# Optimization experiments

Measured on AMD Instinct MI355X. Metric: run time of the kernel, lower is better.

Reference implementation:

```python
import jax, jax.numpy as jnp
import numpy as np

N = 100000
E = 3200000
D_IN = 128
H = 32   # 2 * out_channels
OUT = 16 # out_channels


def _glorot(key, shape):
    lim = np.sqrt(6.0 / (shape[0] + shape[1]))
    return jax.random.uniform(key, shape, jnp.float32, -lim, lim)


def setup_inputs() -> dict:
    key = jax.random.key(0)
    ks = jax.random.split(key, 8)
    x = jax.random.normal(ks[0], (N, D_IN), jnp.float32)
    edge_index = jax.random.randint(ks[1], (2, E), 0, N, jnp.int64)
    W1 = _glorot(ks[2], (D_IN, H));  b1 = jnp.zeros((H,), jnp.float32)
    Wm = _glorot(ks[3], (H, OUT));   bm = jnp.zeros((OUT,), jnp.float32)
    Wv = _glorot(ks[4], (H, 1));     bv = jnp.zeros((1,), jnp.float32)
    return {"x": x, "edge_index": edge_index,
            "W1": W1, "b1": b1, "Wm": Wm, "bm": bm, "Wv": Wv, "bv": bv}


def _gcn_norm(edge_index, n_nodes):
    # add self-loops, then symmetric normalization D^-1/2 (A+I) D^-1/2
    loop = jnp.arange(n_nodes, dtype=edge_index.dtype)
    src = jnp.concatenate([edge_index[0], loop])
    dst = jnp.concatenate([edge_index[1], loop])
    deg = jax.ops.segment_sum(jnp.ones_like(dst, jnp.float32), dst,
                              num_segments=n_nodes)
    dinv = jnp.where(deg > 0, jax.lax.rsqrt(deg), 0.0)
    norm = dinv[src] * dinv[dst]  # [E + N]
    return src, dst, norm


def _gcn_conv(h, W, b, src, dst, norm, n_nodes):
    h = h @ W                                   # [N, out]
    msg = norm[:, None] * h[src]                # gather + scale, [E+N, out]
    out = jax.ops.segment_sum(msg, dst, num_segments=n_nodes)  # scatter-add
    return out + b


def reference(x, edge_index, W1, b1, Wm, bm, Wv, bv):
    src, dst, norm = _gcn_norm(edge_index, N)
    h = jax.nn.relu(_gcn_conv(x, W1, b1, src, dst, norm, N))
    mean = _gcn_conv(h, Wm, bm, src, dst, norm, N)
    mean = mean / jnp.linalg.norm(mean, axis=-1, keepdims=True)
    var = _gcn_conv(h, Wv, bv, src, dst, norm, N)
    var = jax.nn.softplus(var) + 1.0
    return mean, var
```

## Files before the change

### kernel.cpp

```cpp
#include <hip/hip_runtime.h>
#include <math.h>

#define N_NODES   100000
#define N_EDGES   3200000
#define D_IN      128
#define H_DIM     32
#define OUT_DIM   16
#define NB        391
#define B1        512
#define CHUNK     6250
#define NHIST     (NB * B1)
#define SUMS_N    (NHIST / 256)

typedef _Float16 half_t;
typedef __attribute__((ext_vector_type(4))) _Float16 half4;
typedef __attribute__((ext_vector_type(8))) _Float16 half8;


__global__ __launch_bounds__(256) void k_p1_hist(const int* __restrict__ dst,
                                                 int* __restrict__ hist_g) {
    __shared__ int hist[NB];
    int t = threadIdx.x;
    for (int i = t; i < NB; i += 256) hist[i] = 0;
    __syncthreads();
    int base = blockIdx.x * CHUNK;
    for (int k = t; k < CHUNK; k += 256)
        atomicAdd(&hist[dst[base + k] >> 8], 1);
    __syncthreads();
    for (int i = t; i < NB; i += 256) hist_g[i * B1 + blockIdx.x] = hist[i];
}


__global__ __launch_bounds__(256) void k_scanA(const int* __restrict__ hist_g,
                                               int* __restrict__ sums) {
    __shared__ int s[256];
    int t = threadIdx.x;
    s[t] = hist_g[blockIdx.x * 256 + t];
    __syncthreads();
    for (int off = 128; off > 0; off >>= 1) {
        if (t < off) s[t] += s[t + off];
        __syncthreads();
    }
    if (t == 0) sums[blockIdx.x] = s[0];
}

__global__ __launch_bounds__(256) void k_scanB(int* sums) {
    __shared__ int a[256], b[256];
    int t = threadIdx.x;
    int base = t * 4;
    int v0 = (base + 0 < SUMS_N) ? sums[base + 0] : 0;
    int v1 = (base + 1 < SUMS_N) ? sums[base + 1] : 0;
    int v2 = (base + 2 < SUMS_N) ? sums[base + 2] : 0;
    int v3 = (base + 3 < SUMS_N) ? sums[base + 3] : 0;
    int i1 = v0 + v1, i2 = i1 + v2, i3 = i2 + v3;
    a[t] = i3;
    __syncthreads();
    int* cur = a; int* nxt = b;
    for (int off = 1; off < 256; off <<= 1) {
        nxt[t] = cur[t] + ((t >= off) ? cur[t - off] : 0);
        __syncthreads();
        int* tmp = cur; cur = nxt; nxt = tmp;
    }
    int excl = cur[t] - i3;
    if (base + 0 < SUMS_N) sums[base + 0] = excl;
    if (base + 1 < SUMS_N) sums[base + 1] = excl + v0;
    if (base + 2 < SUMS_N) sums[base + 2] = excl + i1;
    if (base + 3 < SUMS_N) sums[base + 3] = excl + i2;
}

__global__ __launch_bounds__(256) void k_scanC(int* hist_g, const int* __restrict__ sums) {
    __shared__ int a[256], b[256];
    int t = threadIdx.x;
    int v = hist_g[blockIdx.x * 256 + t];
    a[t] = v;
    __syncthreads();
    int* cur = a; int* nxt = b;
    for (int off = 1; off < 256; off <<= 1) {
        nxt[t] = cur[t] + ((t >= off) ? cur[t - off] : 0);
        __syncthreads();
        int* tmp = cur; cur = nxt; nxt = tmp;
    }
    hist_g[blockIdx.x * 256 + t] = sums[blockIdx.x] + cur[t] - v;
}


__global__ __launch_bounds__(256) void k_p3(const int* __restrict__ src,
                                            const int* __restrict__ dst,
                                            const int* __restrict__ hist_g,
                                            unsigned int* __restrict__ pairs) {
    __shared__ int cur[NB];
    int t = threadIdx.x;
    for (int i = t; i < NB; i += 256) cur[i] = hist_g[i * B1 + blockIdx.x];
    __syncthreads();
    int base = blockIdx.x * CHUNK;
    for (int k = t; k < CHUNK; k += 256) {
        int e = base + k;
        int d = dst[e];
        int pos = atomicAdd(&cur[d >> 8], 1);
        pairs[pos] = ((unsigned int)(d & 255) << 17) | (unsigned int)src[e];
    }
}


__global__ __launch_bounds__(512) void k_p4(const unsigned int* __restrict__ pairs,
                                            const int* __restrict__ hist_g,
                                            int* __restrict__ csr_src,
                                            int* __restrict__ row_ptr,
                                            float* __restrict__ dinv) {
    __shared__ int cnt[256], a[256], b[256], cur[256];
    int t = threadIdx.x;
    int bk = blockIdx.x;
    int lo = hist_g[bk * B1];
    int hi = (bk + 1 < NB) ? hist_g[(bk + 1) * B1] : N_EDGES;

    if (t < 256) cnt[t] = 0;
    __syncthreads();
    for (int j = lo + t; j < hi; j += 512)
        atomicAdd(&cnt[pairs[j] >> 17], 1);
    __syncthreads();

    if (t < 256) a[t] = cnt[t];
    __syncthreads();
    int* c0 = a; int* c1 = b;
    for (int off = 1; off < 256; off <<= 1) {
        if (t < 256) c1[t] = c0[t] + ((t >= off) ? c0[t - off] : 0);
        __syncthreads();
        int* tmp = c0; c0 = c1; c1 = tmp;
    }
    if (t < 256) {
        int excl = c0[t] - cnt[t];
        cur[t] = lo + excl;
        int node = bk * 256 + t;
        if (node < N_NODES) {
            row_ptr[node] = lo + excl;
            dinv[node] = rsqrtf((float)cnt[t] + 1.0f);
        }
        if (bk == NB - 1 && t == 0) row_ptr[N_NODES] = N_EDGES;
    }
    __syncthreads();

    for (int j = lo + t; j < hi; j += 512) {
        unsigned int p = pairs[j];
        int pos = atomicAdd(&cur[p >> 17], 1);
        csr_src[pos] = (int)(p & 0x1FFFFu);
    }
}


__global__ __launch_bounds__(256) void k_gemm1(const float* __restrict__ x,
                                               const float* __restrict__ W1,
                                               const float* __restrict__ dinv,
                                               half_t* __restrict__ hs) {
    int i = blockIdx.x * 256 + threadIdx.x;
    if (i >= N_NODES) return;

    const float* xr = x + (size_t)i * D_IN;
    float acc[H_DIM];
#pragma unroll
    for (int c = 0; c < H_DIM; ++c) acc[c] = 0.f;

    for (int k0 = 0; k0 < D_IN; k0 += 4) {
        float4 xv = *(const float4*)(xr + k0);
#pragma unroll
        for (int kk = 0; kk < 4; ++kk) {
            float xk = (kk == 0) ? xv.x : (kk == 1) ? xv.y : (kk == 2) ? xv.z : xv.w;
            const float* wr = W1 + (k0 + kk) * H_DIM;
#pragma unroll
            for (int c = 0; c < H_DIM; ++c)
                acc[c] = fmaf(xk, wr[c], acc[c]);
        }
    }

    float di = dinv[i];
    half_t* o = hs + (size_t)i * H_DIM;
#pragma unroll
    for (int c4 = 0; c4 < H_DIM / 4; ++c4) {
        half4 ov;
        ov.x = (half_t)(acc[c4 * 4 + 0] * di);
        ov.y = (half_t)(acc[c4 * 4 + 1] * di);
        ov.z = (half_t)(acc[c4 * 4 + 2] * di);
        ov.w = (half_t)(acc[c4 * 4 + 3] * di);
        *(half4*)(o + c4 * 4) = ov;
    }
}


__global__ __launch_bounds__(256) void k_gather1(const int* __restrict__ row_ptr,
                                                 const int* __restrict__ csr_src,
                                                 const float* __restrict__ dinv,
                                                 const half_t* __restrict__ hs,
                                                 const float* __restrict__ b1,
                                                 half_t* __restrict__ h) {
    int t = blockIdx.x * 256 + threadIdx.x;
    int i = t >> 2, c = t & 3;
    if (i >= N_NODES) return;

    const half8* hp = (const half8*)hs;
    int start = row_ptr[i], end = row_ptr[i + 1];
    half8 sv = hp[(size_t)i * 4 + c];
    float acc[8];
#pragma unroll
    for (int k = 0; k < 8; ++k) acc[k] = (float)sv[k];

    int j = start;
    for (; j + 8 <= end; j += 8) {
        int s0 = csr_src[j + 0], s1 = csr_src[j + 1], s2 = csr_src[j + 2], s3 = csr_src[j + 3];
        int s4 = csr_src[j + 4], s5 = csr_src[j + 5], s6 = csr_src[j + 6], s7 = csr_src[j + 7];
        half8 v0 = hp[(size_t)s0 * 4 + c];
        half8 v1 = hp[(size_t)s1 * 4 + c];
        half8 v2 = hp[(size_t)s2 * 4 + c];
        half8 v3 = hp[(size_t)s3 * 4 + c];
        half8 v4 = hp[(size_t)s4 * 4 + c];
        half8 v5 = hp[(size_t)s5 * 4 + c];
        half8 v6 = hp[(size_t)s6 * 4 + c];
        half8 v7 = hp[(size_t)s7 * 4 + c];
#pragma unroll
        for (int k = 0; k < 8; ++k)
            acc[k] += ((float)v0[k] + (float)v1[k] + (float)v2[k] + (float)v3[k])
                    + ((float)v4[k] + (float)v5[k] + (float)v6[k] + (float)v7[k]);
    }
    for (; j < end; ++j) {
        int s = csr_src[j];
        half8 v = hp[(size_t)s * 4 + c];
#pragma unroll
        for (int k = 0; k < 8; ++k) acc[k] += (float)v[k];
    }

    float di = dinv[i];
    float4 ba = *(const float4*)(b1 + c * 8);
    float4 bb = *(const float4*)(b1 + c * 8 + 4);
    half8 o;
    o[0] = (half_t)fmaxf(di * acc[0] + ba.x, 0.f);
    o[1] = (half_t)fmaxf(di * acc[1] + ba.y, 0.f);
    o[2] = (half_t)fmaxf(di * acc[2] + ba.z, 0.f);
    o[3] = (half_t)fmaxf(di * acc[3] + ba.w, 0.f);
    o[4] = (half_t)fmaxf(di * acc[4] + bb.x, 0.f);
    o[5] = (half_t)fmaxf(di * acc[5] + bb.y, 0.f);
    o[6] = (half_t)fmaxf(di * acc[6] + bb.z, 0.f);
    o[7] = (half_t)fmaxf(di * acc[7] + bb.w, 0.f);
    ((half8*)h)[(size_t)i * 4 + c] = o;
}


__global__ __launch_bounds__(256) void k_gemm2(const half_t* __restrict__ h,
                                               const float* __restrict__ Wm,
                                               const float* __restrict__ Wv,
                                               const float* __restrict__ dinv,
                                               half_t* __restrict__ hmv,
                                               float* __restrict__ varr) {
    int i = blockIdx.x * 256 + threadIdx.x;
    if (i >= N_NODES) return;

    const half4* hp = (const half4*)(h + (size_t)i * H_DIM);
    float acc[OUT_DIM + 1];
#pragma unroll
    for (int c = 0; c <= OUT_DIM; ++c) acc[c] = 0.f;

#pragma unroll
    for (int k4 = 0; k4 < H_DIM / 4; ++k4) {
        half4 v = hp[k4];
#pragma unroll
        for (int kk = 0; kk < 4; ++kk) {
            int k = k4 * 4 + kk;
            float hv = (kk == 0) ? (float)v.x : (kk == 1) ? (float)v.y
                     : (kk == 2) ? (float)v.z : (float)v.w;
            const float* wr = Wm + k * OUT_DIM;
#pragma unroll
            for (int c = 0; c < OUT_DIM; ++c)
                acc[c] = fmaf(hv, wr[c], acc[c]);
            acc[OUT_DIM] = fmaf(hv, Wv[k], acc[OUT_DIM]);
        }
    }

    float di = dinv[i];
    half_t* o = hmv + (size_t)i * OUT_DIM;
#pragma unroll
    for (int c4 = 0; c4 < OUT_DIM / 4; ++c4) {
        half4 ov;
        ov.x = (half_t)(acc[c4 * 4 + 0] * di);
        ov.y = (half_t)(acc[c4 * 4 + 1] * di);
        ov.z = (half_t)(acc[c4 * 4 + 2] * di);
        ov.w = (half_t)(acc[c4 * 4 + 3] * di);
        *(half4*)(o + c4 * 4) = ov;
    }
    varr[i] = acc[OUT_DIM] * di;
}


__global__ __launch_bounds__(256) void k_gather2f(const int* __restrict__ row_ptr,
                                                  const int* __restrict__ csr_src,
                                                  const float* __restrict__ dinv,
                                                  const half_t* __restrict__ hmv,
                                                  const float* __restrict__ varr,
                                                  const float* __restrict__ bm,
                                                  const float* __restrict__ bv,
                                                  float* __restrict__ out) {
    int t = blockIdx.x * 256 + threadIdx.x;
    int i = t >> 2, c = t & 3;
    if (i >= N_NODES) return;

    int start = row_ptr[i], end = row_ptr[i + 1];
    half4 sv = *(const half4*)(hmv + (size_t)i * OUT_DIM + c * 4);
    float a0 = (float)sv.x, a1 = (float)sv.y, a2 = (float)sv.z, a3 = (float)sv.w;
    float va = (c == 0) ? varr[i] : 0.f;

    int j = start;
    for (; j + 4 <= end; j += 4) {
        int s0 = csr_src[j + 0], s1 = csr_src[j + 1], s2 = csr_src[j + 2], s3 = csr_src[j + 3];
        half4 v0 = *(const half4*)(hmv + (size_t)s0 * OUT_DIM + c * 4);
        half4 v1 = *(const half4*)(hmv + (size_t)s1 * OUT_DIM + c * 4);
        half4 v2 = *(const half4*)(hmv + (size_t)s2 * OUT_DIM + c * 4);
        half4 v3 = *(const half4*)(hmv + (size_t)s3 * OUT_DIM + c * 4);
        a0 += (float)v0.x + (float)v1.x + (float)v2.x + (float)v3.x;
        a1 += (float)v0.y + (float)v1.y + (float)v2.y + (float)v3.y;
        a2 += (float)v0.z + (float)v1.z + (float)v2.z + (float)v3.z;
        a3 += (float)v0.w + (float)v1.w + (float)v2.w + (float)v3.w;
        int sc = (c == 0) ? s0 : (c == 1) ? s1 : (c == 2) ? s2 : s3;
        va += varr[sc];
    }
    for (; j < end; ++j) {
        int s = csr_src[j];
        half4 v = *(const half4*)(hmv + (size_t)s * OUT_DIM + c * 4);
        a0 += (float)v.x; a1 += (float)v.y; a2 += (float)v.z; a3 += (float)v.w;
        if (c == 0) va += varr[s];
    }

    float di = dinv[i];
    float4 bb = *(const float4*)(bm + c * 4);
    float r0 = di * a0 + bb.x;
    float r1 = di * a1 + bb.y;
    float r2 = di * a2 + bb.z;
    float r3 = di * a3 + bb.w;
    float ssp = r0 * r0 + r1 * r1 + r2 * r2 + r3 * r3;
    ssp += __shfl_xor(ssp, 1, 4);
    ssp += __shfl_xor(ssp, 2, 4);
    va  += __shfl_xor(va, 1, 4);
    va  += __shfl_xor(va, 2, 4);
    float inv = rsqrtf(ssp);

    float4 o;
    o.x = r0 * inv; o.y = r1 * inv; o.z = r2 * inv; o.w = r3 * inv;
    *(float4*)(out + (size_t)i * OUT_DIM + c * 4) = o;
    if (c == 0) {
        float xv = di * va + bv[0];
        float sp = fmaxf(xv, 0.f) + log1pf(expf(-fabsf(xv)));
        out[(size_t)N_NODES * OUT_DIM + i] = sp + 1.0f;
    }
}


extern "C" void kernel_launch(void* const* d_in, const int* in_sizes, int n_in,
                              void* d_out, int out_size, void* d_ws, size_t ws_size,
                              hipStream_t stream) {
    const float* x  = (const float*)d_in[0];
    const int*   ei = (const int*)d_in[1];
    const float* W1 = (const float*)d_in[2];
    const float* b1 = (const float*)d_in[3];
    const float* Wm = (const float*)d_in[4];
    const float* bm = (const float*)d_in[5];
    const float* Wv = (const float*)d_in[6];
    const float* bv = (const float*)d_in[7];
    float* out = (float*)d_out;

    const int* src = ei;
    const int* dst = ei + N_EDGES;

    int*   wsi     = (int*)d_ws;
    int*   csr_src = wsi;
    int*   row_ptr = csr_src + N_EDGES;
    float* dinv    = (float*)(row_ptr + N_NODES + 1);
    int*   hist_g  = (int*)(dinv + N_NODES);
    int*   sums    = hist_g + NHIST;
    size_t off     = (size_t)(sums + 1024 - wsi);
    off = (off + 3) & ~(size_t)3;
    unsigned int* pairs = (unsigned int*)(wsi + off);
    half_t* hs     = (half_t*)pairs;
    half_t* h      = hs + (size_t)N_NODES * H_DIM;
    half_t* hmv    = h + (size_t)N_NODES * H_DIM;
    float*  varr   = (float*)(hmv + (size_t)N_NODES * OUT_DIM);

    const int B = 256;
    int gN  = (N_NODES + B - 1) / B;
    int gN4 = (N_NODES * 4 + B - 1) / B;

    k_p1_hist<<<B1, B, 0, stream>>>(dst, hist_g);
    k_scanA<<<SUMS_N, B, 0, stream>>>(hist_g, sums);
    k_scanB<<<1, B, 0, stream>>>(sums);
    k_scanC<<<SUMS_N, B, 0, stream>>>(hist_g, sums);
    k_p3<<<B1, B, 0, stream>>>(src, dst, hist_g, pairs);
    k_p4<<<NB, 512, 0, stream>>>(pairs, hist_g, csr_src, row_ptr, dinv);

    k_gemm1<<<gN, B, 0, stream>>>(x, W1, dinv, hs);
    k_gather1<<<gN4, B, 0, stream>>>(row_ptr, csr_src, dinv, hs, b1, h);

    k_gemm2<<<gN, B, 0, stream>>>(h, Wm, Wv, dinv, hmv, varr);
    k_gather2f<<<gN4, B, 0, stream>>>(row_ptr, csr_src, dinv, hmv, varr, bm, bv, out);
}
```

Baseline: 315.0 us.

## Split layer-1 gather by source half for cache locality, double partition blocks

The CSR build now sorts each destination's neighbours into two bins by source index (below or above N/2) and records a mid pointer per row. Layer-1 aggregation is split into two passes, each touching only half of the hs feature table, so each pass's random-access working set is smaller and more likely to stay in cache. A half-precision partial buffer carries the sum between passes. The partition pass also uses twice as many blocks with half the chunk size, and the layer-2 gather loop is unrolled to 8 edges. The costs are an extra kernel launch, an extra read and write of the partial buffer, and one more fp16 rounding of the partial sum.

```diff
diff --git a/kernel.cpp b/kernel.cpp
--- a/kernel.cpp
+++ b/kernel.cpp
@@ -2,15 +2,17 @@
 #include <math.h>
 
 #define N_NODES   100000
+#define N_HALF    50000
 #define N_EDGES   3200000
 #define D_IN      128
 #define H_DIM     32
 #define OUT_DIM   16
 #define NB        391
-#define B1        512
-#define CHUNK     6250
+#define B1        1024
+#define CHUNK     3125
 #define NHIST     (NB * B1)
 #define SUMS_N    (NHIST / 256)
+#define SCANB_PER ((SUMS_N + 255) / 256)
 
 typedef _Float16 half_t;
 typedef __attribute__((ext_vector_type(4))) _Float16 half4;
@@ -47,13 +49,15 @@
 __global__ __launch_bounds__(256) void k_scanB(int* sums) {
     __shared__ int a[256], b[256];
     int t = threadIdx.x;
-    int base = t * 4;
-    int v0 = (base + 0 < SUMS_N) ? sums[base + 0] : 0;
-    int v1 = (base + 1 < SUMS_N) ? sums[base + 1] : 0;
-    int v2 = (base + 2 < SUMS_N) ? sums[base + 2] : 0;
-    int v3 = (base + 3 < SUMS_N) ? sums[base + 3] : 0;
-    int i1 = v0 + v1, i2 = i1 + v2, i3 = i2 + v3;
-    a[t] = i3;
+    int base = t * SCANB_PER;
+    int v[SCANB_PER];
+    int tot = 0;
+#pragma unroll
+    for (int k = 0; k < SCANB_PER; ++k) {
+        v[k] = (base + k < SUMS_N) ? sums[base + k] : 0;
+        tot += v[k];
+    }
+    a[t] = tot;
     __syncthreads();
     int* cur = a; int* nxt = b;
     for (int off = 1; off < 256; off <<= 1) {
@@ -61,11 +65,12 @@
         __syncthreads();
         int* tmp = cur; cur = nxt; nxt = tmp;
     }
-    int excl = cur[t] - i3;
-    if (base + 0 < SUMS_N) sums[base + 0] = excl;
-    if (base + 1 < SUMS_N) sums[base + 1] = excl + v0;
-    if (base + 2 < SUMS_N) sums[base + 2] = excl + i1;
-    if (base + 3 < SUMS_N) sums[base + 3] = excl + i2;
+    int run = cur[t] - tot;
+#pragma unroll
+    for (int k = 0; k < SCANB_PER; ++k) {
+        if (base + k < SUMS_N) sums[base + k] = run;
+        run += v[k];
+    }
 }
 
 __global__ __launch_bounds__(256) void k_scanC(int* hist_g, const int* __restrict__ sums) {
@@ -106,43 +111,53 @@
                                             const int* __restrict__ hist_g,
                                             int* __restrict__ csr_src,
                                             int* __restrict__ row_ptr,
+                                            int* __restrict__ row_mid,
                                             float* __restrict__ dinv) {
-    __shared__ int cnt[256], a[256], b[256], cur[256];
+    __shared__ int cnt[512], a[512], b[512], cur[512];
     int t = threadIdx.x;
     int bk = blockIdx.x;
     int lo = hist_g[bk * B1];
     int hi = (bk + 1 < NB) ? hist_g[(bk + 1) * B1] : N_EDGES;
 
-    if (t < 256) cnt[t] = 0;
-    __syncthreads();
-    for (int j = lo + t; j < hi; j += 512)
-        atomicAdd(&cnt[pairs[j] >> 17], 1);
-    __syncthreads();
-
-    if (t < 256) a[t] = cnt[t];
+    cnt[t] = 0;
+    __syncthreads();
+    for (int j = lo + t; j < hi; j += 512) {
+        unsigned int p = pairs[j];
+        int s = (int)(p & 0x1FFFFu);
+        int bin = (int)((p >> 17) << 1) | (s >= N_HALF);
+        atomicAdd(&cnt[bin], 1);
+    }
+    __syncthreads();
+
+    a[t] = cnt[t];
     __syncthreads();
     int* c0 = a; int* c1 = b;
-    for (int off = 1; off < 256; off <<= 1) {
-        if (t < 256) c1[t] = c0[t] + ((t >= off) ? c0[t - off] : 0);
+    for (int off = 1; off < 512; off <<= 1) {
+        c1[t] = c0[t] + ((t >= off) ? c0[t - off] : 0);
         __syncthreads();
         int* tmp = c0; c0 = c1; c1 = tmp;
     }
-    if (t < 256) {
-        int excl = c0[t] - cnt[t];
-        cur[t] = lo + excl;
-        int node = bk * 256 + t;
-        if (node < N_NODES) {
+    int excl = c0[t] - cnt[t];
+    cur[t] = lo + excl;
+
+    int node = bk * 256 + (t >> 1);
+    if (node < N_NODES) {
+        if ((t & 1) == 0) {
             row_ptr[node] = lo + excl;
-            dinv[node] = rsqrtf((float)cnt[t] + 1.0f);
+            dinv[node] = rsqrtf((float)(cnt[t] + cnt[t + 1]) + 1.0f);
+        } else {
+            row_mid[node] = lo + excl;
         }
-        if (bk == NB - 1 && t == 0) row_ptr[N_NODES] = N_EDGES;
-    }
+    }
+    if (bk == NB - 1 && t == 0) row_ptr[N_NODES] = N_EDGES;
     __syncthreads();
 
     for (int j = lo + t; j < hi; j += 512) {
         unsigned int p = pairs[j];
-        int pos = atomicAdd(&cur[p >> 17], 1);
-        csr_src[pos] = (int)(p & 0x1FFFFu);
+        int s = (int)(p & 0x1FFFFu);
+        int bin = (int)((p >> 17) << 1) | (s >= N_HALF);
+        int pos = atomicAdd(&cur[bin], 1);
+        csr_src[pos] = s;
     }
 }
 
@@ -185,22 +200,71 @@
 }
 
 
-__global__ __launch_bounds__(256) void k_gather1(const int* __restrict__ row_ptr,
-                                                 const int* __restrict__ csr_src,
-                                                 const float* __restrict__ dinv,
-                                                 const half_t* __restrict__ hs,
-                                                 const float* __restrict__ b1,
-                                                 half_t* __restrict__ h) {
+__global__ __launch_bounds__(256) void k_gather1A(const int* __restrict__ row_ptr,
+                                                  const int* __restrict__ row_mid,
+                                                  const int* __restrict__ csr_src,
+                                                  const half_t* __restrict__ hs,
+                                                  half_t* __restrict__ h_part) {
     int t = blockIdx.x * 256 + threadIdx.x;
     int i = t >> 2, c = t & 3;
     if (i >= N_NODES) return;
 
     const half8* hp = (const half8*)hs;
-    int start = row_ptr[i], end = row_ptr[i + 1];
+    int start = row_ptr[i], end = row_mid[i];
+    float acc[8];
+#pragma unroll
+    for (int k = 0; k < 8; ++k) acc[k] = 0.f;
+
+    int j = start;
+    for (; j + 8 <= end; j += 8) {
+        int s0 = csr_src[j + 0], s1 = csr_src[j + 1], s2 = csr_src[j + 2], s3 = csr_src[j + 3];
+        int s4 = csr_src[j + 4], s5 = csr_src[j + 5], s6 = csr_src[j + 6], s7 = csr_src[j + 7];
+        half8 v0 = hp[(size_t)s0 * 4 + c];
+        half8 v1 = hp[(size_t)s1 * 4 + c];
+        half8 v2 = hp[(size_t)s2 * 4 + c];
+        half8 v3 = hp[(size_t)s3 * 4 + c];
+        half8 v4 = hp[(size_t)s4 * 4 + c];
+        half8 v5 = hp[(size_t)s5 * 4 + c];
+        half8 v6 = hp[(size_t)s6 * 4 + c];
+        half8 v7 = hp[(size_t)s7 * 4 + c];
+#pragma unroll
+        for (int k = 0; k < 8; ++k)
+            acc[k] += ((float)v0[k] + (float)v1[k] + (float)v2[k] + (float)v3[k])
+                    + ((float)v4[k] + (float)v5[k] + (float)v6[k] + (float)v7[k]);
+    }
+    for (; j < end; ++j) {
+        int s = csr_src[j];
+        half8 v = hp[(size_t)s * 4 + c];
+#pragma unroll
+        for (int k = 0; k < 8; ++k) acc[k] += (float)v[k];
+    }
+
+    half8 o;
+#pragma unroll
+    for (int k = 0; k < 8; ++k) o[k] = (half_t)acc[k];
+    ((half8*)h_part)[(size_t)i * 4 + c] = o;
+}
+
+
+__global__ __launch_bounds__(256) void k_gather1B(const int* __restrict__ row_ptr,
+                                                  const int* __restrict__ row_mid,
+                                                  const int* __restrict__ csr_src,
+                                                  const float* __restrict__ dinv,
+                                                  const half_t* __restrict__ hs,
+                                                  const half_t* __restrict__ h_part,
+                                                  const float* __restrict__ b1,
+                                                  half_t* __restrict__ h) {
+    int t = blockIdx.x * 256 + threadIdx.x;
+    int i = t >> 2, c = t & 3;
+    if (i >= N_NODES) return;
+
+    const half8* hp = (const half8*)hs;
+    int start = row_mid[i], end = row_ptr[i + 1];
+    half8 pv = ((const half8*)h_part)[(size_t)i * 4 + c];
     half8 sv = hp[(size_t)i * 4 + c];
     float acc[8];
 #pragma unroll
-    for (int k = 0; k < 8; ++k) acc[k] = (float)sv[k];
+    for (int k = 0; k < 8; ++k) acc[k] = (float)pv[k] + (float)sv[k];
 
     int j = start;
     for (; j + 8 <= end; j += 8) {
@@ -305,18 +369,28 @@
     float va = (c == 0) ? varr[i] : 0.f;
 
     int j = start;
-    for (; j + 4 <= end; j += 4) {
+    for (; j + 8 <= end; j += 8) {
         int s0 = csr_src[j + 0], s1 = csr_src[j + 1], s2 = csr_src[j + 2], s3 = csr_src[j + 3];
+        int s4 = csr_src[j + 4], s5 = csr_src[j + 5], s6 = csr_src[j + 6], s7 = csr_src[j + 7];
         half4 v0 = *(const half4*)(hmv + (size_t)s0 * OUT_DIM + c * 4);
         half4 v1 = *(const half4*)(hmv + (size_t)s1 * OUT_DIM + c * 4);
         half4 v2 = *(const half4*)(hmv + (size_t)s2 * OUT_DIM + c * 4);
         half4 v3 = *(const half4*)(hmv + (size_t)s3 * OUT_DIM + c * 4);
-        a0 += (float)v0.x + (float)v1.x + (float)v2.x + (float)v3.x;
-        a1 += (float)v0.y + (float)v1.y + (float)v2.y + (float)v3.y;
-        a2 += (float)v0.z + (float)v1.z + (float)v2.z + (float)v3.z;
-        a3 += (float)v0.w + (float)v1.w + (float)v2.w + (float)v3.w;
-        int sc = (c == 0) ? s0 : (c == 1) ? s1 : (c == 2) ? s2 : s3;
-        va += varr[sc];
+        half4 v4 = *(const half4*)(hmv + (size_t)s4 * OUT_DIM + c * 4);
+        half4 v5 = *(const half4*)(hmv + (size_t)s5 * OUT_DIM + c * 4);
+        half4 v6 = *(const half4*)(hmv + (size_t)s6 * OUT_DIM + c * 4);
+        half4 v7 = *(const half4*)(hmv + (size_t)s7 * OUT_DIM + c * 4);
+        a0 += ((float)v0.x + (float)v1.x + (float)v2.x + (float)v3.x)
+            + ((float)v4.x + (float)v5.x + (float)v6.x + (float)v7.x);
+        a1 += ((float)v0.y + (float)v1.y + (float)v2.y + (float)v3.y)
+            + ((float)v4.y + (float)v5.y + (float)v6.y + (float)v7.y);
+        a2 += ((float)v0.z + (float)v1.z + (float)v2.z + (float)v3.z)
+            + ((float)v4.z + (float)v5.z + (float)v6.z + (float)v7.z);
+        a3 += ((float)v0.w + (float)v1.w + (float)v2.w + (float)v3.w)
+            + ((float)v4.w + (float)v5.w + (float)v6.w + (float)v7.w);
+        int sa = (c == 0) ? s0 : (c == 1) ? s1 : (c == 2) ? s2 : s3;
+        int sb = (c == 0) ? s4 : (c == 1) ? s5 : (c == 2) ? s6 : s7;
+        va += varr[sa] + varr[sb];
     }
     for (; j < end; ++j) {
         int s = csr_src[j];
@@ -368,16 +442,18 @@
     int*   wsi     = (int*)d_ws;
     int*   csr_src = wsi;
     int*   row_ptr = csr_src + N_EDGES;
-    float* dinv    = (float*)(row_ptr + N_NODES + 1);
+    int*   row_mid = row_ptr + N_NODES + 1;
+    float* dinv    = (float*)(row_mid + N_NODES);
     int*   hist_g  = (int*)(dinv + N_NODES);
     int*   sums    = hist_g + NHIST;
-    size_t off     = (size_t)(sums + 1024 - wsi);
+    size_t off     = (size_t)(sums + 2048 - wsi);
     off = (off + 3) & ~(size_t)3;
     unsigned int* pairs = (unsigned int*)(wsi + off);
     half_t* hs     = (half_t*)pairs;
     half_t* h      = hs + (size_t)N_NODES * H_DIM;
     half_t* hmv    = h + (size_t)N_NODES * H_DIM;
     float*  varr   = (float*)(hmv + (size_t)N_NODES * OUT_DIM);
+    half_t* h_part = (half_t*)(varr + N_NODES);
 
     const int B = 256;
     int gN  = (N_NODES + B - 1) / B;
@@ -388,10 +464,11 @@
     k_scanB<<<1, B, 0, stream>>>(sums);
     k_scanC<<<SUMS_N, B, 0, stream>>>(hist_g, sums);
     k_p3<<<B1, B, 0, stream>>>(src, dst, hist_g, pairs);
-    k_p4<<<NB, 512, 0, stream>>>(pairs, hist_g, csr_src, row_ptr, dinv);
+    k_p4<<<NB, 512, 0, stream>>>(pairs, hist_g, csr_src, row_ptr, row_mid, dinv);
 
     k_gemm1<<<gN, B, 0, stream>>>(x, W1, dinv, hs);
-    k_gather1<<<gN4, B, 0, stream>>>(row_ptr, csr_src, dinv, hs, b1, h);
+    k_gather1A<<<gN4, B, 0, stream>>>(row_ptr, row_mid, csr_src, hs, h_part);
+    k_gather1B<<<gN4, B, 0, stream>>>(row_ptr, row_mid, csr_src, dinv, hs, h_part, b1, h);
 
     k_gemm2<<<gN, B, 0, stream>>>(h, Wm, Wv, dinv, hmv, varr);
     k_gather2f<<<gN4, B, 0, stream>>>(row_ptr, csr_src, dinv, hmv, varr, bm, bv, out);
```

Result: no change. 311.1 us (-1.2%).
